# Optimization experiments

Measured on AMD Instinct MI355X. Metric: run time of the kernel, lower is better.

Reference implementation:

```python
import jax, jax.numpy as jnp
import numpy as np
from math import factorial

LMAX = 2
C_DIM = 128
N = 50000
# (l1, l2, l_out) 'uuu' (channel-wise, no weights) instructions, as in the module ([:3])
INSTR = [(2, 2, 0), (1, 2, 1), (1, 1, 2)]


def _f(n):
    return float(factorial(int(n)))


def _su2_cg(j1, m1, j2, m2, j3, m3):
    # Clebsch-Gordan <j1 m1 j2 m2 | j3 m3> (Racah formula), complex SU(2) basis
    if m3 != m1 + m2:
        return 0.0
    vmin = int(max(-j1 + j2 + m3, -j1 + m1, 0))
    vmax = int(min(j2 + j3 + m1, j3 - j1 + j2, j3 + m3))
    pref = ((2 * j3 + 1) * _f(j3 + j1 - j2) * _f(j3 - j1 + j2) * _f(j1 + j2 - j3) / _f(j1 + j2 + j3 + 1)
            * _f(j3 + m3) * _f(j3 - m3) / (_f(j1 - m1) * _f(j1 + m1) * _f(j2 - m2) * _f(j2 + m2))) ** 0.5
    s = 0.0
    for v in range(vmin, vmax + 1):
        s += (-1.0) ** (v + j2 + m2) / _f(v) * _f(j2 + j3 + m1 - v) * _f(j1 - m1 + v) / (
            _f(j3 - j1 + j2 - v) * _f(j3 + m3 - v) * _f(v + j1 - j2 - m3))
    return pref * s


def _q_real_to_complex(l):
    # e3nn change-of-basis from real to complex spherical harmonics
    q = np.zeros((2 * l + 1, 2 * l + 1), dtype=np.complex128)
    for m in range(-l, 0):
        q[l + m, l + abs(m)] = 1.0 / np.sqrt(2)
        q[l + m, l - abs(m)] = -1j / np.sqrt(2)
    q[l, l] = 1.0
    for m in range(1, l + 1):
        q[l + m, l + abs(m)] = (-1) ** m / np.sqrt(2)
        q[l + m, l - abs(m)] = 1j * (-1) ** m / np.sqrt(2)
    return (-1j) ** l * q


def wigner_3j(l1, l2, l3):
    # real-basis Wigner 3j, unit Frobenius norm (e3nn convention)
    Csu2 = np.zeros((2 * l1 + 1, 2 * l2 + 1, 2 * l3 + 1), dtype=np.complex128)
    for i, m1 in enumerate(range(-l1, l1 + 1)):
        for k, m2 in enumerate(range(-l2, l2 + 1)):
            for n, m3 in enumerate(range(-l3, l3 + 1)):
                Csu2[i, k, n] = _su2_cg(l1, m1, l2, m2, l3, m3)
    Q1, Q2, Q3 = _q_real_to_complex(l1), _q_real_to_complex(l2), _q_real_to_complex(l3)
    C = np.einsum('ij,kl,mn,ikn->jlm', Q1, Q2, np.conj(Q3.T), Csu2)
    assert np.abs(C.imag).max() < 1e-7
    C = C.real
    return (C / np.linalg.norm(C)).astype(np.float32)


W3J = {(l1, l2, lo): jnp.asarray(wigner_3j(l1, l2, lo)) for (l1, l2, lo) in INSTR}


def so3_linear(x, W, b):
    # per-degree block-diagonal linear; x: [N, (LMAX+1)^2, Cin], W: [LMAX+1, Cout, Cin], b: [Cout] (l=0 only)
    outs = []
    for l in range(LMAX + 1):
        y = jnp.einsum('nmc,dc->nmd', x[:, l * l:(l + 1) * (l + 1), :], W[l])
        if l == 0:
            y = y + b
        outs.append(y)
    return jnp.concatenate(outs, axis=1)


def tensor_product_uuu(x1, x2):
    # sparse CG tensor product, channel-shared ('uuu'), no path weights
    out = jnp.zeros_like(x1)
    for (l1, l2, lo) in INSTR:
        w3j = W3J[(l1, l2, lo)]
        alpha = float((2 * lo + 1) ** 0.5)  # component normalization
        blk = alpha * jnp.einsum('ijk,nic,njc->nkc', w3j,
                                 x1[:, l1 * l1:(l1 + 1) ** 2, :],
                                 x2[:, l2 * l2:(l2 + 1) ** 2, :])
        out = out.at[:, lo * lo:(lo + 1) ** 2, :].add(blk)
    return out


def setup_inputs() -> dict:
    key = jax.random.key(0)
    ks = jax.random.split(key, 7)
    scale = 1.0 / np.sqrt(C_DIM)
    m_dim = (LMAX + 1) ** 2  # 9
    return {
        'irreps_x': jax.random.normal(ks[0], (N, m_dim, C_DIM), jnp.float32),
        'W_left': jax.random.normal(ks[1], (LMAX + 1, C_DIM, C_DIM), jnp.float32) * scale,
        'b_left': jax.random.normal(ks[2], (C_DIM,), jnp.float32) * scale,
        'W_right': jax.random.normal(ks[3], (LMAX + 1, C_DIM, C_DIM), jnp.float32) * scale,
        'b_right': jax.random.normal(ks[4], (C_DIM,), jnp.float32) * scale,
        'W_final': jax.random.normal(ks[5], (LMAX + 1, C_DIM, C_DIM), jnp.float32) * scale,
        'b_final': jax.random.normal(ks[6], (C_DIM,), jnp.float32) * scale,
    }


def reference(irreps_x, W_left, b_left, W_right, b_right, W_final, b_final):
    xl = so3_linear(irreps_x, W_left, b_left)
    xr = so3_linear(irreps_x, W_right, b_right)
    out = tensor_product_uuu(xl, xr)
    return so3_linear(out, W_final, b_final)  # [N, 9, C]
```

## Files before the change

kernel.cpp:

```cpp
#include <hip/hip_runtime.h>
#include <cmath>
#include <complex>

typedef unsigned short u16;
typedef unsigned int u32;
typedef __bf16 bf16x8 __attribute__((ext_vector_type(8)));
typedef float f32x4 __attribute__((ext_vector_type(4)));

#define CD 128
#define TILE_N 8
#define XS 136
#define LS 132

#define SMEM_TOTAL (72 * XS + 64 * LS + 64 * LS)

struct TPW { float w220[25]; float w121[45]; float w112[45]; };

__device__ __forceinline__ u16 f2b(float f) {
  unsigned u = __float_as_uint(f);
  u += 0x7fffu + ((u >> 16) & 1u);
  return (u16)(u >> 16);
}
__device__ __forceinline__ float b2f(u16 h) {
  return __uint_as_float(((unsigned)h) << 16);
}
__device__ __forceinline__ u32 pack2(float a, float b) {
  return (u32)f2b(a) | ((u32)f2b(b) << 16);
}

__global__ void cvt_weights_kernel(const float* __restrict__ Wl,
                                   const float* __restrict__ Wr,
                                   const float* __restrict__ Wf,
                                   u16* __restrict__ ws) {
  int idx = (blockIdx.x * 256 + threadIdx.x) * 8;
  const float* src; int off;
  if (idx < 49152)      { src = Wl; off = idx; }
  else if (idx < 98304) { src = Wr; off = idx - 49152; }
  else                  { src = Wf; off = idx - 98304; }
  float4 a = *(const float4*)(src + off);
  float4 b = *(const float4*)(src + off + 4);
  uint4 v;
  v.x = pack2(a.x, a.y);
  v.y = pack2(a.z, a.w);
  v.z = pack2(b.x, b.y);
  v.w = pack2(b.z, b.w);
  *(uint4*)(ws + idx) = v;
}

__global__ __launch_bounds__(256, 3)
void fused_kernel(const float* __restrict__ x, const u16* __restrict__ ws,
                  const float* __restrict__ bfin, float* __restrict__ out,
                  int N, TPW tw) {
  __shared__ __align__(16) u16 smem[SMEM_TOTAL];
  u16* bufX = smem;
  u16* sTP  = smem;
  u16* sL   = smem + 72 * XS;
  u16* sR   = smem + 72 * XS + 64 * LS;

  const int tid  = threadIdx.x;
  const int n0   = blockIdx.x * TILE_N;
  const int w    = tid >> 6;
  const int lane = tid & 63;
  const int q    = lane >> 4;
  const int lr   = lane & 15;

  const int mat = w >> 1;
  const int wl  = w & 1;
  u16* dstA = mat ? sR : sL;
  const u16* wsA = ws + mat * 3 * 16384;

  uint4 bfa[2][2][4];
#pragma unroll
  for (int ci = 0; ci < 2; ++ci) {
    int dcol = (wl * 4 + ci) * 16 + lr;
#pragma unroll
    for (int kk = 0; kk < 4; ++kk) {
      bfa[ci][0][kk] = *(const uint4*)(wsA + 16384     + dcol * CD + kk * 32 + q * 8);
      bfa[ci][1][kk] = *(const uint4*)(wsA + 2 * 16384 + dcol * CD + kk * 32 + q * 8);
    }
  }
  const int dc0 = w * 16 + lr;
  const int dc1 = dc0 + 64;
  float bias0 = bfin[dc0];
  float bias1 = bfin[dc1];

#pragma unroll
  for (int it = 0; it < 4; ++it) {
    int e = (it * 256 + tid) * 8;
    int r = e >> 7;
    int c = e & 127;
    int n = n0 + (r & 7);
    if (n >= N) n = N - 1;
    int grow = (n * 9 + 1 + (r >> 3)) * CD + c;
    float4 a = *(const float4*)(x + grow);
    float4 b = *(const float4*)(x + grow + 4);
    uint4 v;
    v.x = pack2(a.x, a.y);
    v.y = pack2(a.z, a.w);
    v.z = pack2(b.x, b.y);
    v.w = pack2(b.z, b.w);
    *(uint4*)(bufX + r * XS + c) = v;
  }
  __syncthreads();

#pragma unroll
  for (int p = 0; p < 2; ++p) {
    if (p == 1) {
#pragma unroll
      for (int ci = 0; ci < 2; ++ci) {
        int dcol = (wl * 4 + 2 + ci) * 16 + lr;
#pragma unroll
        for (int kk = 0; kk < 4; ++kk) {
          bfa[ci][0][kk] = *(const uint4*)(wsA + 16384     + dcol * CD + kk * 32 + q * 8);
          bfa[ci][1][kk] = *(const uint4*)(wsA + 2 * 16384 + dcol * CD + kk * 32 + q * 8);
        }
      }
    }
#pragma unroll
    for (int rt = 0; rt < 5; ++rt) {
      const int l2f   = (rt >= 2) ? 1 : 0;
      const int rows  = l2f ? 40 : 24;
      const int gbase = l2f ? (rt - 2) * 16 : rt * 16;
      const int boff  = l2f ? 24 : 0;
      int ga = gbase + lr; if (ga > rows - 1) ga = rows - 1;
      const int arow = boff + ga;
      uint4 av[4];
#pragma unroll
      for (int kk = 0; kk < 4; ++kk)
        av[kk] = *(const uint4*)(bufX + arow * XS + kk * 32 + q * 8);
#pragma unroll
      for (int ci = 0; ci < 2; ++ci) {
        int dcol = (wl * 4 + 2 * p + ci) * 16 + lr;
        f32x4 acc = {0.f, 0.f, 0.f, 0.f};
#pragma unroll
        for (int kk = 0; kk < 4; ++kk) {
          acc = __builtin_amdgcn_mfma_f32_16x16x32_bf16(
              __builtin_bit_cast(bf16x8, av[kk]),
              __builtin_bit_cast(bf16x8, bfa[ci][l2f][kk]),
              acc, 0, 0, 0);
        }
#pragma unroll
        for (int reg = 0; reg < 4; ++reg) {
          int gg = gbase + q * 4 + reg;
          if (gg < rows) dstA[(boff + gg) * LS + dcol] = f2b(acc[reg]);
        }
      }
    }
  }
  __syncthreads();

#pragma unroll
  for (int iter = 0; iter < 2; ++iter) {
    int id = iter * 256 + tid;
    int cb = (id & 63) * 2;
    int n  = id >> 6;
    const u16* pL = sL + n * LS + cb;
    const u16* pR = sR + n * LS + cb;
    float xl1[2][3], xr1[2][3], xl2[2][5], xr2[2][5];
#pragma unroll
    for (int i = 0; i < 3; ++i) {
      u32 vl = *(const u32*)(pL + i * 8 * LS);
      u32 vr = *(const u32*)(pR + i * 8 * LS);
      xl1[0][i] = b2f((u16)vl); xl1[1][i] = b2f((u16)(vl >> 16));
      xr1[0][i] = b2f((u16)vr); xr1[1][i] = b2f((u16)(vr >> 16));
    }
#pragma unroll
    for (int j = 0; j < 5; ++j) {
      u32 vl = *(const u32*)(pL + (24 + j * 8) * LS);
      u32 vr = *(const u32*)(pR + (24 + j * 8) * LS);
      xl2[0][j] = b2f((u16)vl); xl2[1][j] = b2f((u16)(vl >> 16));
      xr2[0][j] = b2f((u16)vr); xr2[1][j] = b2f((u16)(vr >> 16));
    }
    float o0[2], o1[2][3], o2[2][5];
#pragma unroll
    for (int ch = 0; ch < 2; ++ch) {
      float s0 = 0.f;
#pragma unroll
      for (int i = 0; i < 5; ++i)
#pragma unroll
        for (int j = 0; j < 5; ++j)
          s0 += tw.w220[i * 5 + j] * xl2[ch][i] * xr2[ch][j];
      o0[ch] = s0;
      float a1[3] = {0.f, 0.f, 0.f};
#pragma unroll
      for (int i = 0; i < 3; ++i)
#pragma unroll
        for (int j = 0; j < 5; ++j) {
          float pr = xl1[ch][i] * xr2[ch][j];
#pragma unroll
          for (int k = 0; k < 3; ++k) a1[k] += tw.w121[(i * 5 + j) * 3 + k] * pr;
        }
#pragma unroll
      for (int k = 0; k < 3; ++k) o1[ch][k] = a1[k];
      float a2[5] = {0.f, 0.f, 0.f, 0.f, 0.f};
#pragma unroll
      for (int i = 0; i < 3; ++i)
#pragma unroll
        for (int j = 0; j < 3; ++j) {
          float pr = xl1[ch][i] * xr1[ch][j];
#pragma unroll
          for (int k = 0; k < 5; ++k) a2[k] += tw.w112[(i * 3 + j) * 5 + k] * pr;
        }
#pragma unroll
      for (int k = 0; k < 5; ++k) o2[ch][k] = a2[k];
    }
    u16* pT = sTP + n * XS + cb;
    *(u32*)(pT) = pack2(o0[0], o0[1]);
#pragma unroll
    for (int k = 0; k < 3; ++k) *(u32*)(pT + (1 + k) * 8 * XS) = pack2(o1[0][k], o1[1][k]);
#pragma unroll
    for (int k = 0; k < 5; ++k) *(u32*)(pT + (4 + k) * 8 * XS) = pack2(o2[0][k], o2[1][k]);
  }

  const u16* wsf = ws + 6 * 16384;
  uint4 bc0[4], bc1[4];
#pragma unroll
  for (int kk = 0; kk < 4; ++kk) {
    bc0[kk] = *(const uint4*)(wsf + dc0 * CD + kk * 32 + q * 8);
    bc1[kk] = *(const uint4*)(wsf + dc1 * CD + kk * 32 + q * 8);
  }
  __syncthreads();

#pragma unroll
  for (int l = 0; l < 3; ++l) {
    if (l > 0) {
#pragma unroll
      for (int kk = 0; kk < 4; ++kk) {
        bc0[kk] = *(const uint4*)(wsf + l * 16384 + dc0 * CD + kk * 32 + q * 8);
        bc1[kk] = *(const uint4*)(wsf + l * 16384 + dc1 * CD + kk * 32 + q * 8);
      }
    }
    const int rows   = (l == 0) ? 8 : (l == 1 ? 24 : 40);
    const int soff   = (l == 0) ? 0 : (l == 1 ? 8 : 32);
    const int ntiles = (l == 0) ? 1 : (l == 1 ? 2 : 3);
#pragma unroll
    for (int t = 0; t < 3; ++t) {
      if (t >= ntiles) continue;
      int ga = t * 16 + lr; if (ga > rows - 1) ga = rows - 1;
      const int arow = soff + ga;
      uint4 av[4];
#pragma unroll
      for (int kk = 0; kk < 4; ++kk)
        av[kk] = *(const uint4*)(sTP + arow * XS + kk * 32 + q * 8);
      f32x4 a0 = {0.f, 0.f, 0.f, 0.f};
      f32x4 a1 = {0.f, 0.f, 0.f, 0.f};
#pragma unroll
      for (int kk = 0; kk < 4; ++kk) {
        a0 = __builtin_amdgcn_mfma_f32_16x16x32_bf16(
            __builtin_bit_cast(bf16x8, av[kk]),
            __builtin_bit_cast(bf16x8, bc0[kk]), a0, 0, 0, 0);
        a1 = __builtin_amdgcn_mfma_f32_16x16x32_bf16(
            __builtin_bit_cast(bf16x8, av[kk]),
            __builtin_bit_cast(bf16x8, bc1[kk]), a1, 0, 0, 0);
      }
#pragma unroll
      for (int reg = 0; reg < 4; ++reg) {
        int gg = t * 16 + q * 4 + reg;
        if (gg < rows) {
          int m = l * l + (gg >> 3);
          int n = n0 + (gg & 7);
          if (n < N) {
            float v0 = a0[reg], v1 = a1[reg];
            if (l == 0) { v0 += bias0; v1 += bias1; }
            out[(n * 9 + m) * CD + dc0] = v0;
            out[(n * 9 + m) * CD + dc1] = v1;
          }
        }
      }
    }
  }
}

typedef std::complex<double> cd;

static double factd(int n) { double r = 1.0; for (int i = 2; i <= n; ++i) r *= i; return r; }

static double su2_cg(int j1, int m1, int j2, int m2, int j3, int m3) {
  if (m3 != m1 + m2) return 0.0;
  int vmin = -j1 + j2 + m3; if (-j1 + m1 > vmin) vmin = -j1 + m1; if (0 > vmin) vmin = 0;
  int vmax = j2 + j3 + m1; if (j3 - j1 + j2 < vmax) vmax = j3 - j1 + j2; if (j3 + m3 < vmax) vmax = j3 + m3;
  double pref = std::sqrt((2.0 * j3 + 1.0) * factd(j3 + j1 - j2) * factd(j3 - j1 + j2)
                          * factd(j1 + j2 - j3) / factd(j1 + j2 + j3 + 1)
                          * factd(j3 + m3) * factd(j3 - m3)
                          / (factd(j1 - m1) * factd(j1 + m1) * factd(j2 - m2) * factd(j2 + m2)));
  double s = 0.0;
  for (int v = vmin; v <= vmax; ++v) {
    double sgn = ((v + j2 + m2) & 1) ? -1.0 : 1.0;
    s += sgn / factd(v) * factd(j2 + j3 + m1 - v) * factd(j1 - m1 + v)
         / (factd(j3 - j1 + j2 - v) * factd(j3 + m3 - v) * factd(v + j1 - j2 - m3));
  }
  return pref * s;
}

static void qmat(int l, cd q[5][5]) {
  for (int a = 0; a < 5; ++a) for (int b = 0; b < 5; ++b) q[a][b] = 0.0;
  const double is2 = 1.0 / std::sqrt(2.0);
  for (int m = -l; m < 0; ++m) {
    q[l + m][l - m] = is2;
    q[l + m][l + m] = cd(0.0, -is2);
  }
  q[l][l] = 1.0;
  for (int m = 1; m <= l; ++m) {
    double s = (m & 1) ? -1.0 : 1.0;
    q[l + m][l + m] = s * is2;
    q[l + m][l - m] = cd(0.0, s * is2);
  }
  cd f(1.0, 0.0);
  for (int i = 0; i < l; ++i) f *= cd(0.0, -1.0);
  for (int a = 0; a < 5; ++a) for (int b = 0; b < 5; ++b) q[a][b] *= f;
}

static void wigner3j(int l1, int l2, int l3, double* C) {
  int d1 = 2 * l1 + 1, d2 = 2 * l2 + 1, d3 = 2 * l3 + 1;
  cd Q1[5][5], Q2[5][5], Q3[5][5];
  qmat(l1, Q1); qmat(l2, Q2); qmat(l3, Q3);
  cd Csu2[5][5][5];
  for (int i = 0; i < d1; ++i)
    for (int k = 0; k < d2; ++k)
      for (int n = 0; n < d3; ++n)
        Csu2[i][k][n] = su2_cg(l1, i - l1, l2, k - l2, l3, n - l3);
  double norm = 0.0;
  for (int j = 0; j < d1; ++j)
    for (int lx = 0; lx < d2; ++lx)
      for (int m = 0; m < d3; ++m) {
        cd acc(0.0, 0.0);
        for (int i = 0; i < d1; ++i)
          for (int k = 0; k < d2; ++k)
            for (int n = 0; n < d3; ++n)
              acc += Q1[i][j] * Q2[k][lx] * std::conj(Q3[n][m]) * Csu2[i][k][n];
        C[(j * d2 + lx) * d3 + m] = acc.real();
        norm += acc.real() * acc.real();
      }
  norm = std::sqrt(norm);
  for (int t = 0; t < d1 * d2 * d3; ++t) C[t] /= norm;
}

extern "C" void kernel_launch(void* const* d_in, const int* in_sizes, int n_in,
                              void* d_out, int out_size, void* d_ws, size_t ws_size,
                              hipStream_t stream) {
  const float* x    = (const float*)d_in[0];
  const float* Wl   = (const float*)d_in[1];
  const float* Wr   = (const float*)d_in[3];
  const float* Wf   = (const float*)d_in[5];
  const float* bfin = (const float*)d_in[6];
  float* out = (float*)d_out;
  const int N = in_sizes[0] / (9 * CD);

  TPW tw;
  double c220[25], c121[45], c112[45];
  wigner3j(2, 2, 0, c220);
  wigner3j(1, 2, 1, c121);
  wigner3j(1, 1, 2, c112);
  const double a1 = std::sqrt(3.0), a2 = std::sqrt(5.0);
  for (int i = 0; i < 25; ++i) tw.w220[i] = (float)c220[i];
  for (int i = 0; i < 45; ++i) tw.w121[i] = (float)(a1 * c121[i]);
  for (int i = 0; i < 45; ++i) tw.w112[i] = (float)(a2 * c112[i]);

  u16* ws = (u16*)d_ws;
  cvt_weights_kernel<<<72, 256, 0, stream>>>(Wl, Wr, Wf, ws);
  int grid = (N + TILE_N - 1) / TILE_N;
  fused_kernel<<<grid, 256, 0, stream>>>(x, ws, bfin, out, N, tw);
}
```

Baseline: 502.3 us.

## Halve node tile to 4 and double occupancy target with fewer weight registers

```diff
diff --git a/kernel.cpp b/kernel.cpp
--- a/kernel.cpp
+++ b/kernel.cpp
@@ -8,11 +8,11 @@
 typedef float f32x4 __attribute__((ext_vector_type(4)));
 
 #define CD 128
-#define TILE_N 8
+#define TILE_N 4
 #define XS 136
 #define LS 132
 
-#define SMEM_TOTAL (72 * XS + 64 * LS + 64 * LS)
+#define SMEM_TOTAL (36 * XS + 32 * LS + 32 * LS)
 
 struct TPW { float w220[25]; float w121[45]; float w112[45]; };
 
@@ -47,15 +47,15 @@
   *(uint4*)(ws + idx) = v;
 }
 
-__global__ __launch_bounds__(256, 3)
+__global__ __launch_bounds__(256, 6)
 void fused_kernel(const float* __restrict__ x, const u16* __restrict__ ws,
                   const float* __restrict__ bfin, float* __restrict__ out,
                   int N, TPW tw) {
   __shared__ __align__(16) u16 smem[SMEM_TOTAL];
   u16* bufX = smem;
   u16* sTP  = smem;
-  u16* sL   = smem + 72 * XS;
-  u16* sR   = smem + 72 * XS + 64 * LS;
+  u16* sL   = smem + 36 * XS;
+  u16* sR   = smem + 36 * XS + 32 * LS;
 
   const int tid  = threadIdx.x;
   const int n0   = blockIdx.x * TILE_N;
@@ -69,15 +69,13 @@
   u16* dstA = mat ? sR : sL;
   const u16* wsA = ws + mat * 3 * 16384;
 
-  uint4 bfa[2][2][4];
+  uint4 bf[2][4];
 #pragma unroll
   for (int ci = 0; ci < 2; ++ci) {
     int dcol = (wl * 4 + ci) * 16 + lr;
 #pragma unroll
-    for (int kk = 0; kk < 4; ++kk) {
-      bfa[ci][0][kk] = *(const uint4*)(wsA + 16384     + dcol * CD + kk * 32 + q * 8);
-      bfa[ci][1][kk] = *(const uint4*)(wsA + 2 * 16384 + dcol * CD + kk * 32 + q * 8);
-    }
+    for (int kk = 0; kk < 4; ++kk)
+      bf[ci][kk] = *(const uint4*)(wsA + 16384 + dcol * CD + kk * 32 + q * 8);
   }
   const int dc0 = w * 16 + lr;
   const int dc1 = dc0 + 64;
@@ -85,13 +83,13 @@
   float bias1 = bfin[dc1];
 
 #pragma unroll
-  for (int it = 0; it < 4; ++it) {
+  for (int it = 0; it < 2; ++it) {
     int e = (it * 256 + tid) * 8;
     int r = e >> 7;
     int c = e & 127;
-    int n = n0 + (r & 7);
+    int n = n0 + (r & 3);
     if (n >= N) n = N - 1;
-    int grow = (n * 9 + 1 + (r >> 3)) * CD + c;
+    int grow = (n * 9 + 1 + (r >> 2)) * CD + c;
     float4 a = *(const float4*)(x + grow);
     float4 b = *(const float4*)(x + grow + 4);
     uint4 v;
@@ -110,18 +108,25 @@
       for (int ci = 0; ci < 2; ++ci) {
         int dcol = (wl * 4 + 2 + ci) * 16 + lr;
 #pragma unroll
-        for (int kk = 0; kk < 4; ++kk) {
-          bfa[ci][0][kk] = *(const uint4*)(wsA + 16384     + dcol * CD + kk * 32 + q * 8);
-          bfa[ci][1][kk] = *(const uint4*)(wsA + 2 * 16384 + dcol * CD + kk * 32 + q * 8);
-        }
-      }
-    }
-#pragma unroll
-    for (int rt = 0; rt < 5; ++rt) {
-      const int l2f   = (rt >= 2) ? 1 : 0;
-      const int rows  = l2f ? 40 : 24;
-      const int gbase = l2f ? (rt - 2) * 16 : rt * 16;
-      const int boff  = l2f ? 24 : 0;
+        for (int kk = 0; kk < 4; ++kk)
+          bf[ci][kk] = *(const uint4*)(wsA + 16384 + dcol * CD + kk * 32 + q * 8);
+      }
+    }
+#pragma unroll
+    for (int rt = 0; rt < 3; ++rt) {
+      if (rt == 1) {
+#pragma unroll
+        for (int ci = 0; ci < 2; ++ci) {
+          int dcol = (wl * 4 + 2 * p + ci) * 16 + lr;
+#pragma unroll
+          for (int kk = 0; kk < 4; ++kk)
+            bf[ci][kk] = *(const uint4*)(wsA + 2 * 16384 + dcol * CD + kk * 32 + q * 8);
+        }
+      }
+      const int l2f   = (rt >= 1) ? 1 : 0;
+      const int rows  = l2f ? 20 : 12;
+      const int boff  = l2f ? 12 : 0;
+      const int gbase = (rt == 2) ? 16 : 0;
       int ga = gbase + lr; if (ga > rows - 1) ga = rows - 1;
       const int arow = boff + ga;
       uint4 av[4];
@@ -136,7 +141,7 @@
         for (int kk = 0; kk < 4; ++kk) {
           acc = __builtin_amdgcn_mfma_f32_16x16x32_bf16(
               __builtin_bit_cast(bf16x8, av[kk]),
-              __builtin_bit_cast(bf16x8, bfa[ci][l2f][kk]),
+              __builtin_bit_cast(bf16x8, bf[ci][kk]),
               acc, 0, 0, 0);
         }
 #pragma unroll
@@ -149,25 +154,23 @@
   }
   __syncthreads();
 
-#pragma unroll
-  for (int iter = 0; iter < 2; ++iter) {
-    int id = iter * 256 + tid;
-    int cb = (id & 63) * 2;
-    int n  = id >> 6;
+  {
+    const int cb = (tid & 63) * 2;
+    const int n  = tid >> 6;
     const u16* pL = sL + n * LS + cb;
     const u16* pR = sR + n * LS + cb;
     float xl1[2][3], xr1[2][3], xl2[2][5], xr2[2][5];
 #pragma unroll
     for (int i = 0; i < 3; ++i) {
-      u32 vl = *(const u32*)(pL + i * 8 * LS);
-      u32 vr = *(const u32*)(pR + i * 8 * LS);
+      u32 vl = *(const u32*)(pL + i * 4 * LS);
+      u32 vr = *(const u32*)(pR + i * 4 * LS);
       xl1[0][i] = b2f((u16)vl); xl1[1][i] = b2f((u16)(vl >> 16));
       xr1[0][i] = b2f((u16)vr); xr1[1][i] = b2f((u16)(vr >> 16));
     }
 #pragma unroll
     for (int j = 0; j < 5; ++j) {
-      u32 vl = *(const u32*)(pL + (24 + j * 8) * LS);
-      u32 vr = *(const u32*)(pR + (24 + j * 8) * LS);
+      u32 vl = *(const u32*)(pL + (12 + j * 4) * LS);
+      u32 vr = *(const u32*)(pR + (12 + j * 4) * LS);
       xl2[0][j] = b2f((u16)vl); xl2[1][j] = b2f((u16)(vl >> 16));
       xr2[0][j] = b2f((u16)vr); xr2[1][j] = b2f((u16)(vr >> 16));
     }
@@ -207,9 +210,9 @@
     u16* pT = sTP + n * XS + cb;
     *(u32*)(pT) = pack2(o0[0], o0[1]);
 #pragma unroll
-    for (int k = 0; k < 3; ++k) *(u32*)(pT + (1 + k) * 8 * XS) = pack2(o1[0][k], o1[1][k]);
-#pragma unroll
-    for (int k = 0; k < 5; ++k) *(u32*)(pT + (4 + k) * 8 * XS) = pack2(o2[0][k], o2[1][k]);
+    for (int k = 0; k < 3; ++k) *(u32*)(pT + (1 + k) * 4 * XS) = pack2(o1[0][k], o1[1][k]);
+#pragma unroll
+    for (int k = 0; k < 5; ++k) *(u32*)(pT + (4 + k) * 4 * XS) = pack2(o2[0][k], o2[1][k]);
   }
 
   const u16* wsf = ws + 6 * 16384;
@@ -230,11 +233,11 @@
         bc1[kk] = *(const uint4*)(wsf + l * 16384 + dc1 * CD + kk * 32 + q * 8);
       }
     }
-    const int rows   = (l == 0) ? 8 : (l == 1 ? 24 : 40);
-    const int soff   = (l == 0) ? 0 : (l == 1 ? 8 : 32);
-    const int ntiles = (l == 0) ? 1 : (l == 1 ? 2 : 3);
-#pragma unroll
-    for (int t = 0; t < 3; ++t) {
+    const int rows   = (l == 0) ? 4 : (l == 1 ? 12 : 20);
+    const int soff   = (l == 0) ? 0 : (l == 1 ? 4 : 16);
+    const int ntiles = (l == 2) ? 2 : 1;
+#pragma unroll
+    for (int t = 0; t < 2; ++t) {
       if (t >= ntiles) continue;
       int ga = t * 16 + lr; if (ga > rows - 1) ga = rows - 1;
       const int arow = soff + ga;
@@ -257,8 +260,9 @@
       for (int reg = 0; reg < 4; ++reg) {
         int gg = t * 16 + q * 4 + reg;
         if (gg < rows) {
-          int m = l * l + (gg >> 3);
-          int n = n0 + (gg & 7);
+          int row = soff + gg;
+          int m = row >> 2;
+          int n = n0 + (row & 3);
           if (n < N) {
             float v0 = a0[reg], v1 = a1[reg];
             if (l == 0) { v0 += bias0; v1 += bias1; }
```

Result: slower. 625.4 us (+24.5%).
